# Optimization experiments

Measured on AMD Instinct MI355X. Metric: run time of the kernel, lower is better.

## Reference

```python
import jax, jax.numpy as jnp
import numpy as np

CONF_THRESHOLD = 0.25


def setup_inputs() -> dict:
    key = jax.random.key(0)
    k1, k2, k3 = jax.random.split(key, 3)
    B, A, H, W, V = 16, 3, 128, 128, 85
    output = jax.random.uniform(k1, (B, A, H, W, V), dtype=jnp.float32)
    anchors = jax.random.uniform(k2, (A, 2), dtype=jnp.float32)
    targets = jax.random.uniform(k3, (B, 50, 5), dtype=jnp.float32)
    # make some target rows all-zero padding, as the module expects
    pad_mask = (jnp.arange(50) < 30)[None, :, None]  # first 30 rows valid
    targets = jnp.where(pad_mask, targets, 0.0)
    return {"output": output, "anchors": anchors, "targets": targets}


def reference(output, anchors, targets):
    # output: [B, A, H, W, V] with V = 5 + num_classes
    B = output.shape[0]
    V = output.shape[-1]
    pred = output.reshape(B, -1, V)                      # [B, N, V], N = A*H*W
    box_obj = pred[..., 0:5]                             # x, y, w, h, obj
    cls_scores = pred[..., 5:]                           # [B, N, C]
    cls_id = jnp.argmax(cls_scores, axis=-1).astype(pred.dtype)  # [B, N]
    conf = jnp.max(cls_scores, axis=-1) * pred[..., 4]   # max class prob * objectness
    fused = jnp.concatenate(
        [box_obj, cls_id[..., None], conf[..., None]], axis=-1
    )                                                    # [B, N, 7]
    # confidence filtering expressed as masking (jit-safe: no dynamic shapes)
    keep = conf > CONF_THRESHOLD                         # [B, N]
    pred_out = jnp.where(keep[..., None], fused, 0.0)    # [B, N, 7]
    # target filtering: drop all-zero padding rows (masking instead of slicing)
    valid_t = ~jnp.all(targets == 0.0, axis=-1)          # [B, T]
    target_masked = jnp.where(valid_t[..., None], targets, 0.0)
    return pred_out, target_masked
```

## Files before the change

kernel.cpp:

```cpp
#include <hip/hip_runtime.h>


#define VROW 85
#define NCLS 80
#define OUTW 7
#define ROWS_PER_BLOCK 128
#define CONF_THRESHOLD 0.25f

__global__ __launch_bounds__(ROWS_PER_BLOCK) void yolo_post(
    const float* __restrict__ pred, float* __restrict__ out, int total_rows) {
    __shared__ float lds[ROWS_PER_BLOCK * VROW];

    const int tid = threadIdx.x;
    const long long r0 = (long long)blockIdx.x * ROWS_PER_BLOCK;
    const int rows_here = min(ROWS_PER_BLOCK, total_rows - (int)r0);

    if (rows_here == ROWS_PER_BLOCK) {
        const float4* __restrict__ src =
            reinterpret_cast<const float4*>(pred + (size_t)r0 * VROW);
        float4* dst = reinterpret_cast<float4*>(lds);
        const int nvec = ROWS_PER_BLOCK * VROW / 4;
        #pragma unroll 4
        for (int i = tid; i < nvec; i += ROWS_PER_BLOCK) dst[i] = src[i];
    } else {
        const float* src = pred + (size_t)r0 * VROW;
        const int nflt = rows_here * VROW;
        for (int i = tid; i < nflt; i += ROWS_PER_BLOCK) lds[i] = src[i];
    }
    __syncthreads();

    float o[OUTW];
    if (tid < rows_here) {
        const float* row = lds + tid * VROW;
        const float b0 = row[0], b1 = row[1], b2 = row[2], b3 = row[3];
        const float obj = row[4];
        float best = row[5];
        int besti = 0;
        #pragma unroll
        for (int c = 1; c < NCLS; ++c) {
            const float v = row[5 + c];
            if (v > best) { best = v; besti = c; }
        }
        const float conf = best * obj;
        const bool keep = conf > CONF_THRESHOLD;
        o[0] = keep ? b0 : 0.0f;
        o[1] = keep ? b1 : 0.0f;
        o[2] = keep ? b2 : 0.0f;
        o[3] = keep ? b3 : 0.0f;
        o[4] = keep ? obj : 0.0f;
        o[5] = keep ? (float)besti : 0.0f;
        o[6] = keep ? conf : 0.0f;
    }
    __syncthreads();

    if (tid < rows_here) {
        float* orow = lds + tid * OUTW;
        #pragma unroll
        for (int k = 0; k < OUTW; ++k) orow[k] = o[k];
    }
    __syncthreads();

    if (rows_here == ROWS_PER_BLOCK) {
        const float4* src = reinterpret_cast<const float4*>(lds);
        float4* __restrict__ dst =
            reinterpret_cast<float4*>(out + (size_t)r0 * OUTW);
        const int nvec = ROWS_PER_BLOCK * OUTW / 4;
        for (int i = tid; i < nvec; i += ROWS_PER_BLOCK) dst[i] = src[i];
    } else {
        float* dst = out + (size_t)r0 * OUTW;
        const int nflt = rows_here * OUTW;
        for (int i = tid; i < nflt; i += ROWS_PER_BLOCK) dst[i] = lds[i];
    }
}

__global__ void copy_targets(const float4* __restrict__ src,
                             float4* __restrict__ dst, int nvec) {
    const int i = blockIdx.x * blockDim.x + threadIdx.x;
    if (i < nvec) dst[i] = src[i];
}

extern "C" void kernel_launch(void* const* d_in, const int* in_sizes, int n_in,
                              void* d_out, int out_size, void* d_ws, size_t ws_size,
                              hipStream_t stream) {
    const float* output  = (const float*)d_in[0];
    const float* targets = (const float*)d_in[2];

    float* out = (float*)d_out;
    const int total_rows = in_sizes[0] / VROW;
    const int pred_out_elems = total_rows * OUTW;

    const int nblocks = (total_rows + ROWS_PER_BLOCK - 1) / ROWS_PER_BLOCK;
    yolo_post<<<nblocks, ROWS_PER_BLOCK, 0, stream>>>(output, out, total_rows);

    const int tvec = in_sizes[2] / 4;
    copy_targets<<<(tvec + 255) / 256, 256, 0, stream>>>(
        (const float4*)targets, (float4*)(out + pred_out_elems), tvec);
}
```

Baseline: 363.5 us.

## Load rows via global_load_lds, store outputs directly, fuse target copy

Global-to-shared staging of each 128-row tile now uses the global_load_lds builtin, which writes straight into LDS without going through VGPRs, with a small tail handled by ordinary loads. The LDS-staged output transpose and its two barriers are dropped; each thread writes its 7 output floats directly to global memory. The separate target-copy kernel is folded into block 0 to save a launch. Direct stores are strided by 28 bytes per thread and less coalesced than the old float4 stores, and the target copy only runs if block 0 is a full block.

```diff
diff --git a/kernel.cpp b/kernel.cpp
--- a/kernel.cpp
+++ b/kernel.cpp
@@ -4,32 +4,48 @@
 #define VROW 85
 #define NCLS 80
 #define OUTW 7
-#define ROWS_PER_BLOCK 128
+#define RPB 128
 #define CONF_THRESHOLD 0.25f
 
-__global__ __launch_bounds__(ROWS_PER_BLOCK) void yolo_post(
-    const float* __restrict__ pred, float* __restrict__ out, int total_rows) {
-    __shared__ float lds[ROWS_PER_BLOCK * VROW];
+#define AS1 __attribute__((address_space(1)))
+#define AS3 __attribute__((address_space(3)))
 
-    const int tid = threadIdx.x;
-    const long long r0 = (long long)blockIdx.x * ROWS_PER_BLOCK;
-    const int rows_here = min(ROWS_PER_BLOCK, total_rows - (int)r0);
+__global__ __launch_bounds__(RPB) void yolo_post(
+    const float* __restrict__ pred, float* __restrict__ out, int total_rows,
+    const float4* __restrict__ tgt_src, float4* __restrict__ tgt_dst, int tvec) {
+    __shared__ float lds[RPB * VROW];
 
-    if (rows_here == ROWS_PER_BLOCK) {
-        const float4* __restrict__ src =
-            reinterpret_cast<const float4*>(pred + (size_t)r0 * VROW);
-        float4* dst = reinterpret_cast<float4*>(lds);
-        const int nvec = ROWS_PER_BLOCK * VROW / 4;
-        #pragma unroll 4
-        for (int i = tid; i < nvec; i += ROWS_PER_BLOCK) dst[i] = src[i];
+    const int tid  = threadIdx.x;
+    const int lane = tid & 63;
+    const int wid  = tid >> 6;
+    const long long r0 = (long long)blockIdx.x * RPB;
+    const int rows_here = min(RPB, total_rows - (int)r0);
+
+    if (rows_here == RPB) {
+        const float4* srcv = reinterpret_cast<const float4*>(pred + (size_t)r0 * VROW);
+        const int wbase = wid * 1360;
+        #pragma unroll
+        for (int it = 0; it < 21; ++it) {
+            const int v = wbase + it * 64;
+            __builtin_amdgcn_global_load_lds(
+                (const AS1 void*)(srcv + v + lane),
+                (AS3 void*)((AS3 float*)lds + (size_t)v * 4),
+                16, 0, 0);
+        }
+        if (lane < 16) {
+            const int v = wbase + 1344 + lane;
+            *reinterpret_cast<float4*>(lds + (size_t)v * 4) = srcv[v];
+        }
+        if (blockIdx.x == 0) {
+            for (int i = tid; i < tvec; i += RPB) tgt_dst[i] = tgt_src[i];
+        }
     } else {
         const float* src = pred + (size_t)r0 * VROW;
         const int nflt = rows_here * VROW;
-        for (int i = tid; i < nflt; i += ROWS_PER_BLOCK) lds[i] = src[i];
+        for (int i = tid; i < nflt; i += RPB) lds[i] = src[i];
     }
     __syncthreads();
 
-    float o[OUTW];
     if (tid < rows_here) {
         const float* row = lds + tid * VROW;
         const float b0 = row[0], b1 = row[1], b2 = row[2], b3 = row[3];
@@ -43,40 +59,15 @@
         }
         const float conf = best * obj;
         const bool keep = conf > CONF_THRESHOLD;
-        o[0] = keep ? b0 : 0.0f;
-        o[1] = keep ? b1 : 0.0f;
-        o[2] = keep ? b2 : 0.0f;
-        o[3] = keep ? b3 : 0.0f;
-        o[4] = keep ? obj : 0.0f;
-        o[5] = keep ? (float)besti : 0.0f;
-        o[6] = keep ? conf : 0.0f;
+        float* dst = out + (size_t)(r0 + tid) * OUTW;
+        dst[0] = keep ? b0 : 0.0f;
+        dst[1] = keep ? b1 : 0.0f;
+        dst[2] = keep ? b2 : 0.0f;
+        dst[3] = keep ? b3 : 0.0f;
+        dst[4] = keep ? obj : 0.0f;
+        dst[5] = keep ? (float)besti : 0.0f;
+        dst[6] = keep ? conf : 0.0f;
     }
-    __syncthreads();
-
-    if (tid < rows_here) {
-        float* orow = lds + tid * OUTW;
-        #pragma unroll
-        for (int k = 0; k < OUTW; ++k) orow[k] = o[k];
-    }
-    __syncthreads();
-
-    if (rows_here == ROWS_PER_BLOCK) {
-        const float4* src = reinterpret_cast<const float4*>(lds);
-        float4* __restrict__ dst =
-            reinterpret_cast<float4*>(out + (size_t)r0 * OUTW);
-        const int nvec = ROWS_PER_BLOCK * OUTW / 4;
-        for (int i = tid; i < nvec; i += ROWS_PER_BLOCK) dst[i] = src[i];
-    } else {
-        float* dst = out + (size_t)r0 * OUTW;
-        const int nflt = rows_here * OUTW;
-        for (int i = tid; i < nflt; i += ROWS_PER_BLOCK) dst[i] = lds[i];
-    }
-}
-
-__global__ void copy_targets(const float4* __restrict__ src,
-                             float4* __restrict__ dst, int nvec) {
-    const int i = blockIdx.x * blockDim.x + threadIdx.x;
-    if (i < nvec) dst[i] = src[i];
 }
 
 extern "C" void kernel_launch(void* const* d_in, const int* in_sizes, int n_in,
@@ -89,10 +80,9 @@
     const int total_rows = in_sizes[0] / VROW;
     const int pred_out_elems = total_rows * OUTW;
 
-    const int nblocks = (total_rows + ROWS_PER_BLOCK - 1) / ROWS_PER_BLOCK;
-    yolo_post<<<nblocks, ROWS_PER_BLOCK, 0, stream>>>(output, out, total_rows);
-
+    const int nblocks = (total_rows + RPB - 1) / RPB;
     const int tvec = in_sizes[2] / 4;
-    copy_targets<<<(tvec + 255) / 256, 256, 0, stream>>>(
+    yolo_post<<<nblocks, RPB, 0, stream>>>(
+        output, out, total_rows,
         (const float4*)targets, (float4*)(out + pred_out_elems), tvec);
 }
```

New measurement: 361.1 us. About the same (-0.7%).
